# Kernel optimization log

Hardware: AMD Instinct MI355X
Metric: run time of the kernel (lower is better)

The kernel has to match this reference:

```python
import jax, jax.numpy as jnp
import numpy as np

B, D, H = 4096, 1024, 1024

def _glorot(key, shape):
    fan_in, fan_out = shape
    limit = np.sqrt(6.0 / (fan_in + fan_out))
    return jax.random.uniform(key, shape, jnp.float32, -limit, limit)

def setup_inputs() -> dict:
    key = jax.random.key(0)
    ks = jax.random.split(key, 12)
    inp = {
        'inputs': jax.random.normal(ks[0], (B, D), jnp.float32),
        'h_prev': jax.random.normal(ks[1], (B, H), jnp.float32),
        'c_prev': jax.random.normal(ks[2], (B, H), jnp.float32),
    }
    names = ['f', 'i', 'c', 'o']
    for j, n in enumerate(names):
        inp['W_' + n] = _glorot(ks[3 + 2 * j], (D, H))
        inp['U_' + n] = _glorot(ks[4 + 2 * j], (H, H))
        inp['b_' + n] = jnp.zeros((H,), jnp.float32)
    return inp

def reference(inputs, h_prev, c_prev, W_f, U_f, b_f, W_i, U_i, b_i, W_c, U_c, b_c, W_o, U_o, b_o):
    f_t = jax.nn.sigmoid(inputs @ W_f + h_prev @ U_f + b_f)
    i_t = jax.nn.sigmoid(inputs @ W_i + h_prev @ U_i + b_i)
    c_tilde = jnp.tanh(inputs @ W_c + h_prev @ U_c + b_c)
    c_next = f_t * c_prev + i_t * c_tilde
    o_t = jax.nn.sigmoid(inputs @ W_o + h_prev @ U_o + b_o)
    h_next = o_t * jnp.tanh(c_next)
    return (h_next, c_next)
```

## Files before the change

kernel.cpp:

```cpp
#include <hip/hip_runtime.h>


typedef __attribute__((ext_vector_type(8))) short bfrag8;

__device__ __forceinline__ unsigned int f2bf(float f) {
  unsigned int u = __builtin_bit_cast(unsigned int, f);
  unsigned int r = (u + 0x7fffu + ((u >> 16) & 1u)) >> 16;
  return r & 0xffffu;
}

__global__ __launch_bounds__(256) void prep_x(const float* __restrict__ inputs,
                                              const float* __restrict__ h_prev,
                                              unsigned short* __restrict__ X) {
  int idx = blockIdx.x * 256 + threadIdx.x;
  int b  = idx >> 8;
  int k8 = (idx & 255) * 8;
  const float* src = (k8 < 1024) ? (inputs + (size_t)b * 1024 + k8)
                                 : (h_prev + (size_t)b * 1024 + (k8 - 1024));
  float4 v0 = ((const float4*)src)[0];
  float4 v1 = ((const float4*)src)[1];
  uint4 o;
  o.x = f2bf(v0.x) | (f2bf(v0.y) << 16);
  o.y = f2bf(v0.z) | (f2bf(v0.w) << 16);
  o.z = f2bf(v1.x) | (f2bf(v1.y) << 16);
  o.w = f2bf(v1.z) | (f2bf(v1.w) << 16);
  *(uint4*)(X + (size_t)b * 2048 + k8) = o;
}

__global__ __launch_bounds__(256) void prep_w(
    const float* __restrict__ s0, const float* __restrict__ s1,
    const float* __restrict__ s2, const float* __restrict__ s3,
    const float* __restrict__ s4, const float* __restrict__ s5,
    const float* __restrict__ s6, const float* __restrict__ s7,
    unsigned short* __restrict__ Wct) {
  int blk = blockIdx.x;
  int m = blk >> 8;
  const float* src = (m == 0) ? s0 : (m == 1) ? s1 : (m == 2) ? s2 : (m == 3) ? s3
                   : (m == 4) ? s4 : (m == 5) ? s5 : (m == 6) ? s6 : s7;
  int g = m >> 1, half = m & 1;
  unsigned short* dst = Wct + (size_t)g * 1024 * 2048 + (size_t)half * 1024;
  int t = blk & 255;
  int k0 = (t >> 4) * 64;
  int h0 = (t & 15) * 64;
  __shared__ float lt[64][68];
  int tid = threadIdx.x;
  #pragma unroll
  for (int it = 0; it < 4; ++it) {
    int r  = (tid >> 4) + it * 16;
    int c4 = (tid & 15) * 4;
    float4 v = *(const float4*)(src + (size_t)(k0 + r) * 1024 + h0 + c4);
    lt[r][c4 + 0] = v.x; lt[r][c4 + 1] = v.y; lt[r][c4 + 2] = v.z; lt[r][c4 + 3] = v.w;
  }
  __syncthreads();
  #pragma unroll
  for (int it = 0; it < 4; ++it) {
    int hh  = (tid >> 4) + it * 16;
    int kk4 = (tid & 15) * 4;
    uint2 o;
    o.x = f2bf(lt[kk4 + 0][hh]) | (f2bf(lt[kk4 + 1][hh]) << 16);
    o.y = f2bf(lt[kk4 + 2][hh]) | (f2bf(lt[kk4 + 3][hh]) << 16);
    *(uint2*)(dst + (size_t)(h0 + hh) * 2048 + k0 + kk4) = o;
  }
}


#define FENCE() asm volatile("" ::: "memory")
#define BARRIER() do { FENCE(); __builtin_amdgcn_s_barrier(); FENCE(); } while (0)
#define VMCNT(n) asm volatile("s_waitcnt vmcnt(" #n ")" ::: "memory")
#define LGKM0() asm volatile("s_waitcnt lgkmcnt(0)" ::: "memory")
#define GLOAD16(gp, lp) __builtin_amdgcn_global_load_lds( \
    (const __attribute__((address_space(1))) unsigned int*)(gp), \
    (__attribute__((address_space(3))) unsigned int*)(lp), 16, 0, 0)
#define DSR(dst, addr, off) asm volatile("ds_read_b128 %0, %1 offset:%c2" \
    : "=v"(dst) : "v"(addr), "n"(off))

#define AC "a0","a1","a2","a3","a4","a5","a6","a7","a8","a9","a10","a11","a12","a13","a14","a15", \
 "a16","a17","a18","a19","a20","a21","a22","a23","a24","a25","a26","a27","a28","a29","a30","a31", \
 "a32","a33","a34","a35","a36","a37","a38","a39","a40","a41","a42","a43","a44","a45","a46","a47", \
 "a48","a49","a50","a51","a52","a53","a54","a55","a56","a57","a58","a59","a60","a61","a62","a63", \
 "a64","a65","a66","a67","a68","a69","a70","a71","a72","a73","a74","a75","a76","a77","a78","a79", \
 "a80","a81","a82","a83","a84","a85","a86","a87","a88","a89","a90","a91","a92","a93","a94","a95", \
 "a96","a97","a98","a99","a100","a101","a102","a103","a104","a105","a106","a107","a108","a109","a110","a111", \
 "a112","a113","a114","a115","a116","a117","a118","a119","a120","a121","a122","a123","a124","a125","a126","a127"

#define WZ(n) "v_accvgpr_write_b32 a" #n ", 0\n\t"
#define AINIT() asm volatile( \
 WZ(0)WZ(1)WZ(2)WZ(3)WZ(4)WZ(5)WZ(6)WZ(7)WZ(8)WZ(9)WZ(10)WZ(11)WZ(12)WZ(13)WZ(14)WZ(15) \
 WZ(16)WZ(17)WZ(18)WZ(19)WZ(20)WZ(21)WZ(22)WZ(23)WZ(24)WZ(25)WZ(26)WZ(27)WZ(28)WZ(29)WZ(30)WZ(31) \
 WZ(32)WZ(33)WZ(34)WZ(35)WZ(36)WZ(37)WZ(38)WZ(39)WZ(40)WZ(41)WZ(42)WZ(43)WZ(44)WZ(45)WZ(46)WZ(47) \
 WZ(48)WZ(49)WZ(50)WZ(51)WZ(52)WZ(53)WZ(54)WZ(55)WZ(56)WZ(57)WZ(58)WZ(59)WZ(60)WZ(61)WZ(62)WZ(63) \
 WZ(64)WZ(65)WZ(66)WZ(67)WZ(68)WZ(69)WZ(70)WZ(71)WZ(72)WZ(73)WZ(74)WZ(75)WZ(76)WZ(77)WZ(78)WZ(79) \
 WZ(80)WZ(81)WZ(82)WZ(83)WZ(84)WZ(85)WZ(86)WZ(87)WZ(88)WZ(89)WZ(90)WZ(91)WZ(92)WZ(93)WZ(94)WZ(95) \
 WZ(96)WZ(97)WZ(98)WZ(99)WZ(100)WZ(101)WZ(102)WZ(103)WZ(104)WZ(105)WZ(106)WZ(107)WZ(108)WZ(109)WZ(110)WZ(111) \
 WZ(112)WZ(113)WZ(114)WZ(115)WZ(116)WZ(117)WZ(118)WZ(119)WZ(120)WZ(121)WZ(122)WZ(123)WZ(124)WZ(125)WZ(126)WZ(127) \
 ::: AC)

#define MFMA_ONE(BR, AF, BF) asm volatile( \
    "v_mfma_f32_16x16x32_bf16 a[" BR "], %0, %1, a[" BR "]" \
    :: "v"(AF), "v"(BF) : AC)

#define CLUSTER(B4, B00,B01,B02,B03, B10,B11,B12,B13) do { \
  __builtin_amdgcn_s_setprio(1); \
  MFMA_ONE(B00, afr[0], (B4)[0]); MFMA_ONE(B01, afr[2], (B4)[0]); \
  MFMA_ONE(B02, afr[4], (B4)[0]); MFMA_ONE(B03, afr[6], (B4)[0]); \
  MFMA_ONE(B10, afr[0], (B4)[2]); MFMA_ONE(B11, afr[2], (B4)[2]); \
  MFMA_ONE(B12, afr[4], (B4)[2]); MFMA_ONE(B13, afr[6], (B4)[2]); \
  MFMA_ONE(B00, afr[1], (B4)[1]); MFMA_ONE(B01, afr[3], (B4)[1]); \
  MFMA_ONE(B02, afr[5], (B4)[1]); MFMA_ONE(B03, afr[7], (B4)[1]); \
  MFMA_ONE(B10, afr[1], (B4)[3]); MFMA_ONE(B11, afr[3], (B4)[3]); \
  MFMA_ONE(B12, afr[5], (B4)[3]); MFMA_ONE(B13, afr[7], (B4)[3]); \
  __builtin_amdgcn_s_setprio(0); \
} while (0)

#define CL_00(B4) CLUSTER(B4, "0:3","4:7","8:11","12:15", "32:35","36:39","40:43","44:47")
#define CL_20(B4) CLUSTER(B4, "64:67","68:71","72:75","76:79", "96:99","100:103","104:107","108:111")
#define CL_24(B4) CLUSTER(B4, "80:83","84:87","88:91","92:95", "112:115","116:119","120:123","124:127")
#define CL_04(B4) CLUSTER(B4, "16:19","20:23","24:27","28:31", "48:51","52:55","56:59","60:63")

#define READ_A8(arr, BUF, RB) do { \
  DSR(arr[0], aA0, (BUF)*16384 + (RB)*128 + 0);    \
  DSR(arr[1], aA1, (BUF)*16384 + (RB)*128 + 0);    \
  DSR(arr[2], aA0, (BUF)*16384 + (RB)*128 + 2048); \
  DSR(arr[3], aA1, (BUF)*16384 + (RB)*128 + 2048); \
  DSR(arr[4], aA0, (BUF)*16384 + (RB)*128 + 4096); \
  DSR(arr[5], aA1, (BUF)*16384 + (RB)*128 + 4096); \
  DSR(arr[6], aA0, (BUF)*16384 + (RB)*128 + 6144); \
  DSR(arr[7], aA1, (BUF)*16384 + (RB)*128 + 6144); \
} while (0)

#define READ_B4(arr, BUF, CB) do { \
  DSR(arr[0], aB0, (BUF)*16384 + (CB)*128 + 0);    \
  DSR(arr[1], aB1, (BUF)*16384 + (CB)*128 + 0);    \
  DSR(arr[2], aB0, (BUF)*16384 + (CB)*128 + 2048); \
  DSR(arr[3], aB1, (BUF)*16384 + (CB)*128 + 2048); \
} while (0)

#define STAGE_A(BUF, H, kt) do { int _kb = ((kt) < 32 ? (kt) : 31) * 64; \
  GLOAD16(pA0 + (size_t)(H) * 262144 + _kb, smem + (H)*32768 + (BUF)*16384 + stbase); \
  GLOAD16(pA1 + (size_t)(H) * 262144 + _kb, smem + (H)*32768 + (BUF)*16384 + stbase + 1024); \
} while (0)

#define STAGE_B0(BUF, kt) do { int _kb = ((kt) < 32 ? (kt) : 31) * 64; \
  GLOAD16(pB00 + _kb, smem + 65536 + (BUF)*16384 + stbase); \
  GLOAD16(pB01 + _kb, smem + 65536 + (BUF)*16384 + stbase + 1024); \
} while (0)

#define STAGE_B1(BUF, kt) do { int _kb = ((kt) < 32 ? (kt) : 31) * 64; \
  GLOAD16(pB10 + _kb, smem + 98304 + (BUF)*16384 + stbase); \
  GLOAD16(pB11 + _kb, smem + 98304 + (BUF)*16384 + stbase + 1024); \
} while (0)

#define ARD(X, RS) asm volatile("v_accvgpr_read_b32 %0, " RS : "=v"(X))

#define EPI_M(Mi, F0,F1,F2,F3, I0,I1,I2,I3, C0,C1,C2,C3, O0,O1,O2,O3) do { \
  float pf[4], pi[4], pc[4], po[4]; \
  ARD(pf[0],F0); ARD(pf[1],F1); ARD(pf[2],F2); ARD(pf[3],F3); \
  ARD(pi[0],I0); ARD(pi[1],I1); ARD(pi[2],I2); ARD(pi[3],I3); \
  ARD(pc[0],C0); ARD(pc[1],C1); ARD(pc[2],C2); ARD(pc[3],C3); \
  ARD(po[0],O0); ARD(po[1],O1); ARD(po[2],O2); ARD(po[3],O3); \
  _Pragma("unroll") for (int j = 0; j < 4; ++j) { \
    const int b = rbw + (Mi) * 16 + q * 4 + j; \
    float xf = pf[j] + Bgf, xi = pi[j] + Bgi, xc = pc[j] + Bgc, xo = po[j] + Bgo; \
    float fg = 1.f / (1.f + __expf(-xf)); \
    float ig = 1.f / (1.f + __expf(-xi)); \
    float ct = 2.f / (1.f + __expf(-2.f * xc)) - 1.f; \
    float og = 1.f / (1.f + __expf(-xo)); \
    float cn = fg * c_prev[(size_t)b * 1024 + hcol] + ig * ct; \
    float hn = og * (2.f / (1.f + __expf(-2.f * cn)) - 1.f); \
    out[(size_t)b * 1024 + hcol] = hn; \
    out[(size_t)4194304 + (size_t)b * 1024 + hcol] = cn; \
  } \
} while (0)

__global__ __launch_bounds__(512, 2) void lstm_gemm(
    const unsigned short* __restrict__ X, const unsigned short* __restrict__ Wct,
    const float* __restrict__ c_prev,
    const float* __restrict__ bfv, const float* __restrict__ biv,
    const float* __restrict__ bcv, const float* __restrict__ bov,
    float* __restrict__ out) {
  extern __shared__ __align__(16) char smem[];
  const int tid = threadIdx.x;
  const int lane = tid & 63, w = tid >> 6;
  const int u = lane & 15, q = (lane >> 4) & 3;
  const int wm = w >> 2, wn = w & 3;

  const int bid = blockIdx.x;
  const int swz = (bid & 7) * 32 + (bid >> 3);
  const int h0 = (swz & 15) * 64;
  const int row0 = (swz >> 4) * 256;

  const unsigned lds0 = (unsigned)(size_t)((__attribute__((address_space(3))) char*)smem);

  const int sw0 = (q ^ (u & 7)) << 4;
  const int sw1 = ((q + 4) ^ (u & 7)) << 4;
  const unsigned aA0 = lds0 + wm * 32768 + u * 128 + sw0;
  const unsigned aA1 = lds0 + wm * 32768 + u * 128 + sw1;
  const unsigned aB0 = lds0 + 65536 + (wn >> 1) * 32768 + ((wn & 1) * 64 + u) * 128 + sw0;
  const unsigned aB1 = lds0 + 65536 + (wn >> 1) * 32768 + ((wn & 1) * 64 + u) * 128 + sw1;

  const int stbase = w * 2048 + lane * 16;
  const int rA0 = w * 16 + (lane >> 3), rA1 = rA0 + 8;
  const int ssA = (lane & 7) ^ (rA0 & 7);
  const unsigned short* pA0 = X + (size_t)(row0 + rA0) * 2048 + ssA * 8;
  const unsigned short* pA1 = X + (size_t)(row0 + rA1) * 2048 + ssA * 8;
  auto wrow = [&](int C) { return (((C >> 4) & 3) << 10) + h0 + ((C >> 6) << 4) + (C & 15); };
  const unsigned short* pB00 = Wct + (size_t)wrow(rA0) * 2048 + ssA * 8;
  const unsigned short* pB01 = Wct + (size_t)wrow(rA1) * 2048 + ssA * 8;
  const unsigned short* pB10 = Wct + (size_t)wrow(128 + rA0) * 2048 + ssA * 8;
  const unsigned short* pB11 = Wct + (size_t)wrow(128 + rA1) * 2048 + ssA * 8;

  AINIT();

  bfrag8 afr[8], bh[4], bl0[4], bl1[4];

  STAGE_B0(0, 0); STAGE_B1(0, 0); STAGE_A(0, 0, 0); STAGE_A(0, 1, 0);
  STAGE_B0(1, 1); STAGE_B1(1, 1);
  VMCNT(4);
  BARRIER();
  READ_B4(bl0, 0, 0);

  #pragma unroll 1
  for (int t = 0; t < 16; ++t) {
    const int kt1 = 2 * t + 1, kt2 = 2 * t + 2, kt3 = 2 * t + 3;
    READ_A8(afr, 0, 0);
    STAGE_A(1, 0, kt1);
    BARRIER(); LGKM0();
    CL_00(bl0);
    READ_B4(bh, 0, 32);
    STAGE_A(1, 1, kt1);
    BARRIER(); LGKM0();
    CL_20(bh);
    READ_A8(afr, 0, 64);
    VMCNT(4);
    BARRIER(); LGKM0();
    CL_24(bh);
    READ_B4(bl1, 1, 0);
    STAGE_B0(0, kt2);
    STAGE_B1(0, kt2);
    VMCNT(4);
    BARRIER(); LGKM0();
    CL_04(bl0);
    READ_A8(afr, 1, 0);
    STAGE_A(0, 0, kt2);
    BARRIER(); LGKM0();
    CL_00(bl1);
    READ_B4(bh, 1, 32);
    STAGE_A(0, 1, kt2);
    BARRIER(); LGKM0();
    CL_20(bh);
    READ_A8(afr, 1, 64);
    VMCNT(4);
    BARRIER(); LGKM0();
    CL_24(bh);
    READ_B4(bl0, 0, 0);
    STAGE_B0(1, kt3);
    STAGE_B1(1, kt3);
    VMCNT(4);
    BARRIER(); LGKM0();
    CL_04(bl1);
  }
  VMCNT(0);
  asm volatile("s_nop 7\n\ts_nop 7");

  const int hcol = h0 + wn * 16 + u;
  const float Bgf = bfv[hcol], Bgi = biv[hcol], Bgc = bcv[hcol], Bgo = bov[hcol];
  const int rbw = row0 + wm * 128;
  EPI_M(0, "a0","a1","a2","a3",     "a32","a33","a34","a35",
           "a64","a65","a66","a67", "a96","a97","a98","a99");
  EPI_M(1, "a4","a5","a6","a7",     "a36","a37","a38","a39",
           "a68","a69","a70","a71", "a100","a101","a102","a103");
  EPI_M(2, "a8","a9","a10","a11",   "a40","a41","a42","a43",
           "a72","a73","a74","a75", "a104","a105","a106","a107");
  EPI_M(3, "a12","a13","a14","a15", "a44","a45","a46","a47",
           "a76","a77","a78","a79", "a108","a109","a110","a111");
  EPI_M(4, "a16","a17","a18","a19", "a48","a49","a50","a51",
           "a80","a81","a82","a83", "a112","a113","a114","a115");
  EPI_M(5, "a20","a21","a22","a23", "a52","a53","a54","a55",
           "a84","a85","a86","a87", "a116","a117","a118","a119");
  EPI_M(6, "a24","a25","a26","a27", "a56","a57","a58","a59",
           "a88","a89","a90","a91", "a120","a121","a122","a123");
  EPI_M(7, "a28","a29","a30","a31", "a60","a61","a62","a63",
           "a92","a93","a94","a95", "a124","a125","a126","a127");
}

extern "C" void kernel_launch(void* const* d_in, const int* in_sizes, int n_in,
                              void* d_out, int out_size, void* d_ws, size_t ws_size,
                              hipStream_t stream) {
  const float* inputs = (const float*)d_in[0];
  const float* h_prev = (const float*)d_in[1];
  const float* c_prev = (const float*)d_in[2];
  const float* Wf = (const float*)d_in[3];
  const float* Uf = (const float*)d_in[4];
  const float* bf = (const float*)d_in[5];
  const float* Wi = (const float*)d_in[6];
  const float* Ui = (const float*)d_in[7];
  const float* bi = (const float*)d_in[8];
  const float* Wc = (const float*)d_in[9];
  const float* Uc = (const float*)d_in[10];
  const float* bc = (const float*)d_in[11];
  const float* Wo = (const float*)d_in[12];
  const float* Uo = (const float*)d_in[13];
  const float* bo = (const float*)d_in[14];
  float* out = (float*)d_out;

  unsigned short* X   = (unsigned short*)d_ws;
  unsigned short* Wct = X + (size_t)4096 * 2048;

  (void)hipFuncSetAttribute(reinterpret_cast<const void*>(lstm_gemm),
                            hipFuncAttributeMaxDynamicSharedMemorySize, 131072);

  prep_x<<<4096, 256, 0, stream>>>(inputs, h_prev, X);
  prep_w<<<2048, 256, 0, stream>>>(Wf, Uf, Wi, Ui, Wc, Uc, Wo, Uo, Wct);
  lstm_gemm<<<256, 512, 131072, stream>>>(X, Wct, c_prev, bf, bi, bc, bo, out);
}
```

Baseline: 87.33 us.

## Restructure LDS layout and MFMA schedule to prefetch fragments across clusters

Reorganizes the LDS buffers so each K-stage holds A and B halves contiguously, and rewrites the main loop to double-buffer A and B register fragments. Waits change from lgkmcnt(0) to partial counts, so LDS reads for the next MFMA cluster are in flight while the current one runs. Clusters now cover 16 accumulators over 4 A by 4 B fragments, replacing 8 A by 2 B. The extra buffers raise VGPR pressure, the full vmcnt(0) waits may stall on global loads, and the partial lgkmcnt values must exactly match how many DS reads are outstanding.

```diff
diff --git a/kernel.cpp b/kernel.cpp
--- a/kernel.cpp
+++ b/kernel.cpp
@@ -67,7 +67,7 @@
 #define FENCE() asm volatile("" ::: "memory")
 #define BARRIER() do { FENCE(); __builtin_amdgcn_s_barrier(); FENCE(); } while (0)
 #define VMCNT(n) asm volatile("s_waitcnt vmcnt(" #n ")" ::: "memory")
-#define LGKM0() asm volatile("s_waitcnt lgkmcnt(0)" ::: "memory")
+#define LGKM(n) asm volatile("s_waitcnt lgkmcnt(" #n ")" ::: "memory")
 #define GLOAD16(gp, lp) __builtin_amdgcn_global_load_lds( \
     (const __attribute__((address_space(1))) unsigned int*)(gp), \
     (__attribute__((address_space(3))) unsigned int*)(lp), 16, 0, 0)
@@ -99,55 +99,50 @@
     "v_mfma_f32_16x16x32_bf16 a[" BR "], %0, %1, a[" BR "]" \
     :: "v"(AF), "v"(BF) : AC)
 
-#define CLUSTER(B4, B00,B01,B02,B03, B10,B11,B12,B13) do { \
+#define CLUSTER16(A4, B4, R00,R01,R02,R03, R10,R11,R12,R13, R20,R21,R22,R23, R30,R31,R32,R33) do { \
   __builtin_amdgcn_s_setprio(1); \
-  MFMA_ONE(B00, afr[0], (B4)[0]); MFMA_ONE(B01, afr[2], (B4)[0]); \
-  MFMA_ONE(B02, afr[4], (B4)[0]); MFMA_ONE(B03, afr[6], (B4)[0]); \
-  MFMA_ONE(B10, afr[0], (B4)[2]); MFMA_ONE(B11, afr[2], (B4)[2]); \
-  MFMA_ONE(B12, afr[4], (B4)[2]); MFMA_ONE(B13, afr[6], (B4)[2]); \
-  MFMA_ONE(B00, afr[1], (B4)[1]); MFMA_ONE(B01, afr[3], (B4)[1]); \
-  MFMA_ONE(B02, afr[5], (B4)[1]); MFMA_ONE(B03, afr[7], (B4)[1]); \
-  MFMA_ONE(B10, afr[1], (B4)[3]); MFMA_ONE(B11, afr[3], (B4)[3]); \
-  MFMA_ONE(B12, afr[5], (B4)[3]); MFMA_ONE(B13, afr[7], (B4)[3]); \
+  MFMA_ONE(R00, (A4)[0], (B4)[0]); MFMA_ONE(R01, (A4)[1], (B4)[0]); \
+  MFMA_ONE(R02, (A4)[2], (B4)[0]); MFMA_ONE(R03, (A4)[3], (B4)[0]); \
+  MFMA_ONE(R10, (A4)[0], (B4)[1]); MFMA_ONE(R11, (A4)[1], (B4)[1]); \
+  MFMA_ONE(R12, (A4)[2], (B4)[1]); MFMA_ONE(R13, (A4)[3], (B4)[1]); \
+  MFMA_ONE(R20, (A4)[0], (B4)[2]); MFMA_ONE(R21, (A4)[1], (B4)[2]); \
+  MFMA_ONE(R22, (A4)[2], (B4)[2]); MFMA_ONE(R23, (A4)[3], (B4)[2]); \
+  MFMA_ONE(R30, (A4)[0], (B4)[3]); MFMA_ONE(R31, (A4)[1], (B4)[3]); \
+  MFMA_ONE(R32, (A4)[2], (B4)[3]); MFMA_ONE(R33, (A4)[3], (B4)[3]); \
   __builtin_amdgcn_s_setprio(0); \
 } while (0)
 
-#define CL_00(B4) CLUSTER(B4, "0:3","4:7","8:11","12:15", "32:35","36:39","40:43","44:47")
-#define CL_20(B4) CLUSTER(B4, "64:67","68:71","72:75","76:79", "96:99","100:103","104:107","108:111")
-#define CL_24(B4) CLUSTER(B4, "80:83","84:87","88:91","92:95", "112:115","116:119","120:123","124:127")
-#define CL_04(B4) CLUSTER(B4, "16:19","20:23","24:27","28:31", "48:51","52:55","56:59","60:63")
-
-#define READ_A8(arr, BUF, RB) do { \
-  DSR(arr[0], aA0, (BUF)*16384 + (RB)*128 + 0);    \
-  DSR(arr[1], aA1, (BUF)*16384 + (RB)*128 + 0);    \
-  DSR(arr[2], aA0, (BUF)*16384 + (RB)*128 + 2048); \
-  DSR(arr[3], aA1, (BUF)*16384 + (RB)*128 + 2048); \
-  DSR(arr[4], aA0, (BUF)*16384 + (RB)*128 + 4096); \
-  DSR(arr[5], aA1, (BUF)*16384 + (RB)*128 + 4096); \
-  DSR(arr[6], aA0, (BUF)*16384 + (RB)*128 + 6144); \
-  DSR(arr[7], aA1, (BUF)*16384 + (RB)*128 + 6144); \
-} while (0)
-
-#define READ_B4(arr, BUF, CB) do { \
-  DSR(arr[0], aB0, (BUF)*16384 + (CB)*128 + 0);    \
-  DSR(arr[1], aB1, (BUF)*16384 + (CB)*128 + 0);    \
-  DSR(arr[2], aB0, (BUF)*16384 + (CB)*128 + 2048); \
-  DSR(arr[3], aB1, (BUF)*16384 + (CB)*128 + 2048); \
+#define CL_MH0(A4, B4) CLUSTER16(A4, B4, \
+  "0:3","4:7","8:11","12:15", "32:35","36:39","40:43","44:47", \
+  "64:67","68:71","72:75","76:79", "96:99","100:103","104:107","108:111")
+#define CL_MH1(A4, B4) CLUSTER16(A4, B4, \
+  "16:19","20:23","24:27","28:31", "48:51","52:55","56:59","60:63", \
+  "80:83","84:87","88:91","92:95", "112:115","116:119","120:123","124:127")
+
+#define READ_A4(arr, BUF, MH, ABASE) do { \
+  DSR(arr[0], ABASE, (BUF)*32768 + (MH)*8192 + 0);    \
+  DSR(arr[1], ABASE, (BUF)*32768 + (MH)*8192 + 2048); \
+  DSR(arr[2], ABASE, (BUF)*32768 + (MH)*8192 + 4096); \
+  DSR(arr[3], ABASE, (BUF)*32768 + (MH)*8192 + 6144); \
+} while (0)
+
+#define READ_B4N(arr, BUF, BBASE) do { \
+  DSR(arr[0], BBASE, (BUF)*32768 + 0);    \
+  DSR(arr[1], BBASE, (BUF)*32768 + 2048); \
+  DSR(arr[2], BBASE, (BUF)*32768 + 4096); \
+  DSR(arr[3], BBASE, (BUF)*32768 + 6144); \
 } while (0)
 
 #define STAGE_A(BUF, H, kt) do { int _kb = ((kt) < 32 ? (kt) : 31) * 64; \
-  GLOAD16(pA0 + (size_t)(H) * 262144 + _kb, smem + (H)*32768 + (BUF)*16384 + stbase); \
-  GLOAD16(pA1 + (size_t)(H) * 262144 + _kb, smem + (H)*32768 + (BUF)*16384 + stbase + 1024); \
-} while (0)
-
-#define STAGE_B0(BUF, kt) do { int _kb = ((kt) < 32 ? (kt) : 31) * 64; \
-  GLOAD16(pB00 + _kb, smem + 65536 + (BUF)*16384 + stbase); \
-  GLOAD16(pB01 + _kb, smem + 65536 + (BUF)*16384 + stbase + 1024); \
-} while (0)
-
-#define STAGE_B1(BUF, kt) do { int _kb = ((kt) < 32 ? (kt) : 31) * 64; \
-  GLOAD16(pB10 + _kb, smem + 98304 + (BUF)*16384 + stbase); \
-  GLOAD16(pB11 + _kb, smem + 98304 + (BUF)*16384 + stbase + 1024); \
+  GLOAD16(pA0 + (size_t)(H) * 262144 + _kb, smem + (BUF)*32768 + (H)*16384 + stbase); \
+  GLOAD16(pA1 + (size_t)(H) * 262144 + _kb, smem + (BUF)*32768 + (H)*16384 + stbase + 1024); \
+} while (0)
+
+#define STAGE_B(BUF, kt) do { int _kb = ((kt) < 32 ? (kt) : 31) * 64; \
+  GLOAD16(pB00 + _kb, smem + 65536 + (BUF)*32768 + stbase); \
+  GLOAD16(pB01 + _kb, smem + 65536 + (BUF)*32768 + stbase + 1024); \
+  GLOAD16(pB10 + _kb, smem + 65536 + (BUF)*32768 + 16384 + stbase); \
+  GLOAD16(pB11 + _kb, smem + 65536 + (BUF)*32768 + 16384 + stbase + 1024); \
 } while (0)
 
 #define ARD(X, RS) asm volatile("v_accvgpr_read_b32 %0, " RS : "=v"(X))
@@ -193,10 +188,10 @@
 
   const int sw0 = (q ^ (u & 7)) << 4;
   const int sw1 = ((q + 4) ^ (u & 7)) << 4;
-  const unsigned aA0 = lds0 + wm * 32768 + u * 128 + sw0;
-  const unsigned aA1 = lds0 + wm * 32768 + u * 128 + sw1;
-  const unsigned aB0 = lds0 + 65536 + (wn >> 1) * 32768 + ((wn & 1) * 64 + u) * 128 + sw0;
-  const unsigned aB1 = lds0 + 65536 + (wn >> 1) * 32768 + ((wn & 1) * 64 + u) * 128 + sw1;
+  const unsigned aA0 = lds0 + wm * 16384 + u * 128 + sw0;
+  const unsigned aA1 = lds0 + wm * 16384 + u * 128 + sw1;
+  const unsigned aB0 = lds0 + 65536 + (wn * 64 + u) * 128 + sw0;
+  const unsigned aB1 = lds0 + 65536 + (wn * 64 + u) * 128 + sw1;
 
   const int stbase = w * 2048 + lane * 16;
   const int rA0 = w * 16 + (lane >> 3), rA1 = rA0 + 8;
@@ -211,55 +206,55 @@
 
   AINIT();
 
-  bfrag8 afr[8], bh[4], bl0[4], bl1[4];
-
-  STAGE_B0(0, 0); STAGE_B1(0, 0); STAGE_A(0, 0, 0); STAGE_A(0, 1, 0);
-  STAGE_B0(1, 1); STAGE_B1(1, 1);
+  bfrag8 Ab0[4], Ab1[4], Bb0[4], Bb1[4];
+
+  STAGE_A(0, 0, 0); STAGE_A(0, 1, 0);
+  STAGE_B(0, 0);
+  STAGE_B(1, 1);
   VMCNT(4);
   BARRIER();
-  READ_B4(bl0, 0, 0);
+  READ_A4(Ab0, 0, 0, aA0);
+  READ_B4N(Bb0, 0, aB0);
 
   #pragma unroll 1
   for (int t = 0; t < 16; ++t) {
     const int kt1 = 2 * t + 1, kt2 = 2 * t + 2, kt3 = 2 * t + 3;
-    READ_A8(afr, 0, 0);
-    STAGE_A(1, 0, kt1);
-    BARRIER(); LGKM0();
-    CL_00(bl0);
-    READ_B4(bh, 0, 32);
-    STAGE_A(1, 1, kt1);
-    BARRIER(); LGKM0();
-    CL_20(bh);
-    READ_A8(afr, 0, 64);
-    VMCNT(4);
-    BARRIER(); LGKM0();
-    CL_24(bh);
-    READ_B4(bl1, 1, 0);
-    STAGE_B0(0, kt2);
-    STAGE_B1(0, kt2);
-    VMCNT(4);
-    BARRIER(); LGKM0();
-    CL_04(bl0);
-    READ_A8(afr, 1, 0);
-    STAGE_A(0, 0, kt2);
-    BARRIER(); LGKM0();
-    CL_00(bl1);
-    READ_B4(bh, 1, 32);
-    STAGE_A(0, 1, kt2);
-    BARRIER(); LGKM0();
-    CL_20(bh);
-    READ_A8(afr, 1, 64);
-    VMCNT(4);
-    BARRIER(); LGKM0();
-    CL_24(bh);
-    READ_B4(bl0, 0, 0);
-    STAGE_B0(1, kt3);
-    STAGE_B1(1, kt3);
-    VMCNT(4);
-    BARRIER(); LGKM0();
-    CL_04(bl1);
+    READ_A4(Ab1, 0, 1, aA0);
+    STAGE_A(1, 0, kt1); STAGE_A(1, 1, kt1);
+    BARRIER(); LGKM(4);
+    CL_MH0(Ab0, Bb0);
+    READ_A4(Ab0, 0, 0, aA1);
+    READ_B4N(Bb1, 0, aB1);
+    BARRIER(); LGKM(8);
+    CL_MH1(Ab1, Bb0);
+    READ_A4(Ab1, 0, 1, aA1);
+    VMCNT(0);
+    BARRIER(); LGKM(4);
+    CL_MH0(Ab0, Bb1);
+    READ_A4(Ab0, 1, 0, aA0);
+    READ_B4N(Bb0, 1, aB0);
+    STAGE_B(0, kt2);
+    BARRIER(); LGKM(8);
+    CL_MH1(Ab1, Bb1);
+    READ_A4(Ab1, 1, 1, aA0);
+    STAGE_A(0, 0, kt2); STAGE_A(0, 1, kt2);
+    BARRIER(); LGKM(4);
+    CL_MH0(Ab0, Bb0);
+    READ_A4(Ab0, 1, 0, aA1);
+    READ_B4N(Bb1, 1, aB1);
+    BARRIER(); LGKM(8);
+    CL_MH1(Ab1, Bb0);
+    READ_A4(Ab1, 1, 1, aA1);
+    VMCNT(0);
+    BARRIER(); LGKM(4);
+    CL_MH0(Ab0, Bb1);
+    READ_A4(Ab0, 0, 0, aA0);
+    READ_B4N(Bb0, 0, aB0);
+    STAGE_B(1, kt3);
+    BARRIER(); LGKM(8);
+    CL_MH1(Ab1, Bb1);
   }
-  VMCNT(0);
+  VMCNT(0); LGKM(0);
   asm volatile("s_nop 7\n\ts_nop 7");
 
   const int hcol = h0 + wn * 16 + u;
```

Measured after the change: 87.58 us. Within noise of the previous version (+0.3%).
